# Kernel optimization log

Hardware: AMD Instinct MI355X
Metric: run time of the kernel (lower is better)

The kernel has to match this reference:

```python
import jax, jax.numpy as jnp
import numpy as np

INPUT_DIM = 1024
HIDDEN_DIM = 64   # per-head dim
NUM_HEADS = 16
PROJ = HIDDEN_DIM * NUM_HEADS  # 1024


def setup_inputs() -> dict:
    key = jax.random.key(0)
    ks = jax.random.split(key, 9)
    s = 1.0 / np.sqrt(INPUT_DIM)
    x = jax.random.normal(ks[0], (4, 2048, INPUT_DIM), dtype=jnp.float32)
    # Linear weights stored [in, out] (math-equivalent to torch's W.T)
    Wq = jax.random.uniform(ks[1], (INPUT_DIM, PROJ), jnp.float32, -s, s)
    bq = jax.random.uniform(ks[2], (PROJ,), jnp.float32, -s, s)
    Wk = jax.random.uniform(ks[3], (INPUT_DIM, PROJ), jnp.float32, -s, s)
    bk = jax.random.uniform(ks[4], (PROJ,), jnp.float32, -s, s)
    Wv = jax.random.uniform(ks[5], (INPUT_DIM, PROJ), jnp.float32, -s, s)
    bv = jax.random.uniform(ks[6], (PROJ,), jnp.float32, -s, s)
    sf = 1.0 / np.sqrt(PROJ)
    Wf = jax.random.uniform(ks[7], (PROJ, HIDDEN_DIM), jnp.float32, -sf, sf)
    bf = jax.random.uniform(ks[8], (HIDDEN_DIM,), jnp.float32, -sf, sf)
    return {"x": x, "Wq": Wq, "bq": bq, "Wk": Wk, "bk": bk,
            "Wv": Wv, "bv": bv, "Wf": Wf, "bf": bf}


def reference(x, Wq, bq, Wk, bk, Wv, bv, Wf, bf):
    B, S, _ = x.shape
    def split_heads(t):  # [B,S,H*D] -> [B,H,S,D]
        return t.reshape(B, S, NUM_HEADS, HIDDEN_DIM).transpose(0, 2, 1, 3)
    q = split_heads(x @ Wq + bq)
    k = split_heads(x @ Wk + bk)
    v = split_heads(x @ Wv + bv)
    scale = 1.0 / jnp.sqrt(jnp.float32(HIDDEN_DIM))
    scores = jnp.einsum('bhqd,bhkd->bhqk', q, k) * scale  # [B,H,S,S]
    weights = jax.nn.softmax(scores, axis=-1)
    ctx = jnp.einsum('bhqk,bhkd->bhqd', weights, v)
    ctx = ctx.transpose(0, 2, 1, 3).reshape(B, S, PROJ)
    return ctx @ Wf + bf  # [B,S,HIDDEN_DIM]
```

## Files before the change

kernel.cpp:

```cpp
#include <hip/hip_runtime.h>
#include <math.h>

#define S_LEN 2048
#define NH 16
#define HD 64
#define DMODEL 1024
#define BATCH 4
#define M_TOT (BATCH * S_LEN)

typedef __attribute__((ext_vector_type(8))) short bf16x8;
typedef __attribute__((ext_vector_type(4))) float f32x4;

#define CK 0.18033688f

__device__ __forceinline__ unsigned short f2bf_rne(float f) {
    unsigned u = __float_as_uint(f);
    u += 0x7fffu + ((u >> 16) & 1u);
    return (unsigned short)(u >> 16);
}

__device__ __forceinline__ void gld16(unsigned short* lds, const unsigned short* g) {
    __builtin_amdgcn_global_load_lds(
        (const __attribute__((address_space(1))) void*)g,
        (__attribute__((address_space(3))) void*)lds, 16, 0, 0);
}

__global__ __launch_bounds__(256) void cvt_fused(
    const float* __restrict__ x,
    const float* __restrict__ Wq, const float* __restrict__ Wk,
    const float* __restrict__ Wv, const float* __restrict__ Wf,
    unsigned short* __restrict__ xb, unsigned short* __restrict__ WT)
{
    const int z = blockIdx.z;
    const int tid = threadIdx.x;

    if (z < 4) {
        if (z == 3 && blockIdx.x > 0) return;
        const float* W = (z == 0) ? Wq : (z == 1) ? Wk : (z == 2) ? Wv : Wf;
        const int ncol = (z == 3) ? 64 : DMODEL;
        unsigned short* out = WT + (size_t)z * DMODEL * DMODEL;

        __shared__ float Lt[64][65];
        const int r0 = blockIdx.y * 64;
        const int c0 = blockIdx.x * 64;

        #pragma unroll
        for (int p = 0; p < 4; p++) {
            int row = (tid >> 4) + p * 16;
            int c4 = (tid & 15) * 4;
            float4 v = *(const float4*)(W + (size_t)(r0 + row) * ncol + c0 + c4);
            Lt[row][c4 + 0] = v.x; Lt[row][c4 + 1] = v.y;
            Lt[row][c4 + 2] = v.z; Lt[row][c4 + 3] = v.w;
        }
        __syncthreads();
        #pragma unroll
        for (int p = 0; p < 4; p++) {
            int nr = (tid >> 4) + p * 16;
            int kc = (tid & 15) * 4;
            unsigned short t[4];
            #pragma unroll
            for (int j = 0; j < 4; j++) t[j] = f2bf_rne(Lt[kc + j][nr]);
            *(uint2*)(out + (size_t)(c0 + nr) * DMODEL + r0 + kc) = *(uint2*)t;
        }
    } else {
        const int zz = z - 4;
        const int gtid = (blockIdx.y * 16 + blockIdx.x) * 256 + tid;
        #pragma unroll
        for (int it = 0; it < 2; it++) {
            #pragma unroll
            for (int k = 0; k < 4; k++) {
                size_t i = ((size_t)((zz * 8 + it * 4 + k) * 65536) + gtid) * 4;
                float4 v = *(const float4*)(x + i);
                unsigned short t[4];
                t[0] = f2bf_rne(v.x); t[1] = f2bf_rne(v.y);
                t[2] = f2bf_rne(v.z); t[3] = f2bf_rne(v.w);
                *(uint2*)(xb + i) = *(uint2*)t;
            }
        }
    }
}

__global__ __launch_bounds__(512) void qkv_fused_mfma(
    const unsigned short* __restrict__ xb,
    const unsigned short* __restrict__ WT,
    const float* __restrict__ bq, const float* __restrict__ bk,
    const float* __restrict__ bv,
    unsigned short* __restrict__ Qb, unsigned short* __restrict__ Kb,
    unsigned short* __restrict__ Vtb)
{
    __shared__ __align__(16) unsigned short Ws[3][24 * 512];

    const int lin = blockIdx.x;
    const int xcd = lin & 7;
    const int s   = lin >> 3;
    const int rb  = xcd * 4 + (s & 3);
    const int ocb = s >> 2;

    const int tid = threadIdx.x;
    const int lane = tid & 63, w = tid >> 6;
    const int quad = lane >> 4, l15 = lane & 15;

    const int R0  = rb * 256;
    const int OC0 = ocb * 64;

    const unsigned short* gW0 = WT +
        (size_t)(OC0 + (w >> 1) * 16 + l15) * DMODEL + (w & 1) * 32 + quad * 8;
    const unsigned short* gW1 = gW0 + (size_t)DMODEL * DMODEL;
    const unsigned short* gW2 = gW1 + (size_t)DMODEL * DMODEL;
    const unsigned short* gx0 = xb +
        (size_t)(R0 + w * 32 + l15) * DMODEL + quad * 8;
    const unsigned short* gx1 = gx0 + (size_t)16 * DMODEL;

    f32x4 acc[3][4][2];
    #pragma unroll
    for (int z = 0; z < 3; z++)
        #pragma unroll
        for (int i = 0; i < 4; i++)
            #pragma unroll
            for (int j = 0; j < 2; j++)
                #pragma unroll
                for (int c = 0; c < 4; c++) acc[z][i][j][c] = 0.f;

#define QKV_STAGEW(BUF, K)  do {                                       \
        gld16(Ws[BUF] + (0 * 8 + w) * 512, gW0 + (K));                 \
        gld16(Ws[BUF] + (1 * 8 + w) * 512, gW1 + (K));                 \
        gld16(Ws[BUF] + (2 * 8 + w) * 512, gW2 + (K));                 \
    } while (0)

#define QKV_LOADX(XF, K)  do {                                         \
        XF[0][0] = *(const bf16x8*)(gx0 + (K));                        \
        XF[0][1] = *(const bf16x8*)(gx0 + (K) + 32);                   \
        XF[1][0] = *(const bf16x8*)(gx1 + (K));                        \
        XF[1][1] = *(const bf16x8*)(gx1 + (K) + 32);                   \
    } while (0)

#define QKV_COMPUTE(BUF, XF)  do {                                     \
        _Pragma("unroll")                                              \
        for (int sl = 0; sl < 2; sl++) {                               \
            _Pragma("unroll")                                          \
            for (int z = 0; z < 3; z++) {                              \
                bf16x8 af[4];                                          \
                _Pragma("unroll")                                      \
                for (int i = 0; i < 4; i++)                            \
                    af[i] = *(const bf16x8*)&Ws[BUF][(z * 8 + i * 2 + sl) * 512 + lane * 8]; \
                if (z != 2) {                                          \
                    _Pragma("unroll")                                  \
                    for (int i = 0; i < 4; i++)                        \
                        _Pragma("unroll")                              \
                        for (int j = 0; j < 2; j++)                    \
                            acc[z][i][j] = __builtin_amdgcn_mfma_f32_16x16x32_bf16( \
                                af[i], XF[j][sl], acc[z][i][j], 0, 0, 0); \
                } else {                                               \
                    _Pragma("unroll")                                  \
                    for (int i = 0; i < 4; i++)                        \
                        _Pragma("unroll")                              \
                        for (int j = 0; j < 2; j++)                    \
                            acc[2][i][j] = __builtin_amdgcn_mfma_f32_16x16x32_bf16( \
                                XF[j][sl], af[i], acc[2][i][j], 0, 0, 0); \
                }                                                      \
            }                                                          \
        }                                                              \
    } while (0)

    bf16x8 xA[2][2], xB[2][2];

    QKV_STAGEW(0, 0);
    QKV_LOADX(xA, 0);
    QKV_STAGEW(1, 64);

    int b0 = 0;
    #pragma unroll 1
    for (int tt = 0; tt < 16; tt += 2) {
        const int b1 = (b0 + 1 == 3) ? 0 : b0 + 1;
        const int b2 = (b1 + 1 == 3) ? 0 : b1 + 1;

        asm volatile("s_waitcnt vmcnt(3)" ::: "memory");
        __builtin_amdgcn_s_barrier();
        if (tt < 15) QKV_LOADX(xB, (tt + 1) * 64);
        if (tt < 14) QKV_STAGEW(b2, (tt + 2) * 64);
        QKV_COMPUTE(b0, xA);

        if (tt < 14) asm volatile("s_waitcnt vmcnt(3)" ::: "memory");
        else         asm volatile("s_waitcnt vmcnt(0)" ::: "memory");
        __builtin_amdgcn_s_barrier();
        if (tt < 14) QKV_LOADX(xA, (tt + 2) * 64);
        if (tt < 13) QKV_STAGEW(b0, (tt + 3) * 64);
        QKV_COMPUTE(b1, xB);

        b0 = b2;
    }
#undef QKV_STAGEW
#undef QKV_LOADX
#undef QKV_COMPUTE

    #pragma unroll
    for (int z = 0; z < 2; z++) {
        unsigned short* out = (z == 0) ? Qb : Kb;
        const float* bias = (z == 0) ? bq : bk;
        const float qs = (z == 0) ? CK : 1.0f;
        #pragma unroll
        for (int i = 0; i < 4; i++) {
            int oc = OC0 + i * 16 + quad * 4;
            float4 bv4 = *(const float4*)&bias[oc];
            #pragma unroll
            for (int j = 0; j < 2; j++) {
                int row = R0 + w * 32 + j * 16 + l15;
                unsigned short t4[4];
                t4[0] = f2bf_rne((acc[z][i][j][0] + bv4.x) * qs);
                t4[1] = f2bf_rne((acc[z][i][j][1] + bv4.y) * qs);
                t4[2] = f2bf_rne((acc[z][i][j][2] + bv4.z) * qs);
                t4[3] = f2bf_rne((acc[z][i][j][3] + bv4.w) * qs);
                *(uint2*)(out + (size_t)row * DMODEL + oc) = *(uint2*)t4;
            }
        }
    }
    {
        const int b = R0 >> 11;
        const int sbase = (R0 & 2047) + w * 32;
        #pragma unroll
        for (int i = 0; i < 4; i++) {
            int oc = OC0 + i * 16 + l15;
            float bvv = bv[oc];
            #pragma unroll
            for (int j = 0; j < 2; j++) {
                int sq = sbase + j * 16 + quad * 4;
                unsigned short t4[4];
                t4[0] = f2bf_rne(acc[2][i][j][0] + bvv);
                t4[1] = f2bf_rne(acc[2][i][j][1] + bvv);
                t4[2] = f2bf_rne(acc[2][i][j][2] + bvv);
                t4[3] = f2bf_rne(acc[2][i][j][3] + bvv);
                *(uint2*)(Vtb + (size_t)(b * DMODEL + oc) * S_LEN + sq) = *(uint2*)t4;
            }
        }
    }
}

__global__ __launch_bounds__(512, 4) void flash_attn_mfma(
    const unsigned short* __restrict__ Qg,
    const unsigned short* __restrict__ Kg,
    const unsigned short* __restrict__ Vtg,
    unsigned short* __restrict__ ctxb)
{
    __shared__ __align__(16) unsigned short Ks[16 * 512];
    __shared__ __align__(16) unsigned short Vs[16 * 512];
    __shared__ __align__(16) unsigned short Ps[16 * 512];

    const int tid  = threadIdx.x;
    const int lane = tid & 63, w = tid >> 6;
    const int quad = lane >> 4, l15 = lane & 15;

    const int lin = blockIdx.x;
    const int xcd = lin & 7;
    const int s   = lin >> 3;
    const int bh  = xcd + 8 * (s >> 3);
    const int qblk = s & 7;
    const int b = bh >> 4, h = bh & 15;
    const int r0 = qblk * 256;

    bf16x8 qf[2][2];
    #pragma unroll
    for (int nt = 0; nt < 2; nt++)
        #pragma unroll
        for (int ds = 0; ds < 2; ds++)
            qf[nt][ds] = *(const bf16x8*)(Qg +
                (size_t)(b * S_LEN + r0 + w * 32 + nt * 16 + l15) * DMODEL +
                h * HD + ds * 32 + quad * 8);

    const int sw = w & 3;
    const unsigned short* gK = Kg +
        (size_t)(b * S_LEN + sw * 32 + l15) * DMODEL + h * HD + quad * 8;
    const unsigned short* gV = Vtg +
        ((size_t)(bh * HD + sw * 16 + l15)) * S_LEN + quad * 8;

    f32x4 O[2][4], lsum[2];
    #pragma unroll
    for (int rt = 0; rt < 2; rt++) {
        #pragma unroll
        for (int c = 0; c < 4; c++) lsum[rt][c] = 0.f;
        #pragma unroll
        for (int dt = 0; dt < 4; dt++)
            #pragma unroll
            for (int c = 0; c < 4; c++) O[rt][dt][c] = 0.f;
    }

    f32x4 zero4;
    #pragma unroll
    for (int c = 0; c < 4; c++) zero4[c] = 0.f;
    bf16x8 ones;
    #pragma unroll
    for (int c = 0; c < 8; c++) ones[c] = (short)0x3F80;

    for (int st = 0; st < S_LEN / 128; st++) {
        __syncthreads();
        if (w < 4) {
            gld16(Ks + (w * 4 + 0) * 512, gK);
            gld16(Ks + (w * 4 + 1) * 512, gK + 32);
            gld16(Ks + (w * 4 + 2) * 512, gK + (size_t)16 * DMODEL);
            gld16(Ks + (w * 4 + 3) * 512, gK + (size_t)16 * DMODEL + 32);
            gK += (size_t)128 * DMODEL;
        } else {
            gld16(Vs + (sw * 4 + 0) * 512, gV);
            gld16(Vs + (sw * 4 + 1) * 512, gV + 32);
            gld16(Vs + (sw * 4 + 2) * 512, gV + 64);
            gld16(Vs + (sw * 4 + 3) * 512, gV + 96);
            gV += 128;
        }
        __syncthreads();

        #pragma unroll
        for (int r = 0; r < 4; r++) {
            f32x4 sc[2][2];
            {
                bf16x8 kf0 = *(const bf16x8*)&Ks[((r * 2 + 0) * 2 + 0) * 512 + lane * 8];
                bf16x8 kf1 = *(const bf16x8*)&Ks[((r * 2 + 1) * 2 + 0) * 512 + lane * 8];
                sc[0][0] = __builtin_amdgcn_mfma_f32_16x16x32_bf16(kf0, qf[0][0], zero4, 0, 0, 0);
                sc[0][1] = __builtin_amdgcn_mfma_f32_16x16x32_bf16(kf0, qf[1][0], zero4, 0, 0, 0);
                sc[1][0] = __builtin_amdgcn_mfma_f32_16x16x32_bf16(kf1, qf[0][0], zero4, 0, 0, 0);
                sc[1][1] = __builtin_amdgcn_mfma_f32_16x16x32_bf16(kf1, qf[1][0], zero4, 0, 0, 0);
                kf0 = *(const bf16x8*)&Ks[((r * 2 + 0) * 2 + 1) * 512 + lane * 8];
                kf1 = *(const bf16x8*)&Ks[((r * 2 + 1) * 2 + 1) * 512 + lane * 8];
                sc[0][0] = __builtin_amdgcn_mfma_f32_16x16x32_bf16(kf0, qf[0][1], sc[0][0], 0, 0, 0);
                sc[0][1] = __builtin_amdgcn_mfma_f32_16x16x32_bf16(kf0, qf[1][1], sc[0][1], 0, 0, 0);
                sc[1][0] = __builtin_amdgcn_mfma_f32_16x16x32_bf16(kf1, qf[0][1], sc[1][0], 0, 0, 0);
                sc[1][1] = __builtin_amdgcn_mfma_f32_16x16x32_bf16(kf1, qf[1][1], sc[1][1], 0, 0, 0);
            }

            #pragma unroll
            for (int nt = 0; nt < 2; nt++) {
                #pragma unroll
                for (int mt = 0; mt < 2; mt++) {
                    unsigned u[4];
                    #pragma unroll
                    for (int c = 0; c < 4; c++)
                        u[c] = __float_as_uint(__builtin_amdgcn_exp2f(sc[mt][nt][c]));
                    uint2 pk;
                    pk.x = __builtin_amdgcn_perm(u[1], u[0], 0x07060302u);
                    pk.y = __builtin_amdgcn_perm(u[3], u[2], 0x07060302u);
                    int off = (w * 2 + nt) * 512 + (mt * 2 + (quad >> 1)) * 128 +
                              l15 * 8 + (quad & 1) * 4;
                    *(uint2*)&Ps[off] = pk;
                }
            }

            bf16x8 pf0 = *(const bf16x8*)&Ps[(w * 2 + 0) * 512 + lane * 8];
            bf16x8 pf1 = *(const bf16x8*)&Ps[(w * 2 + 1) * 512 + lane * 8];
            lsum[0] = __builtin_amdgcn_mfma_f32_16x16x32_bf16(pf0, ones, lsum[0], 0, 0, 0);
            lsum[1] = __builtin_amdgcn_mfma_f32_16x16x32_bf16(pf1, ones, lsum[1], 0, 0, 0);
            #pragma unroll
            for (int dt = 0; dt < 4; dt++) {
                bf16x8 vf = *(const bf16x8*)&Vs[(dt * 4 + r) * 512 + lane * 8];
                O[0][dt] = __builtin_amdgcn_mfma_f32_16x16x32_bf16(pf0, vf, O[0][dt], 0, 0, 0);
                O[1][dt] = __builtin_amdgcn_mfma_f32_16x16x32_bf16(pf1, vf, O[1][dt], 0, 0, 0);
            }
        }
    }

    const size_t srow = (size_t)(b * S_LEN + r0 + w * 32);
    #pragma unroll
    for (int rt = 0; rt < 2; rt++) {
        #pragma unroll
        for (int reg = 0; reg < 4; reg++) {
            float li = 1.0f / lsum[rt][reg];
            size_t rowoff = (srow + rt * 16 + quad * 4 + reg) * DMODEL + h * HD + l15;
            #pragma unroll
            for (int dt = 0; dt < 4; dt++)
                ctxb[rowoff + dt * 16] = f2bf_rne(O[rt][dt][reg] * li);
        }
    }
}

__global__ __launch_bounds__(512) void out_proj_mfma(
    const unsigned short* __restrict__ ctxb,
    const unsigned short* __restrict__ WfT,
    const float* __restrict__ bfb,
    float* __restrict__ out)
{
    __shared__ float Red[8 * 1024];

    const int tid = threadIdx.x;
    const int lane = tid & 63, w = tid >> 6;
    const int quad = lane >> 4, l15 = lane & 15;
    const int m0 = blockIdx.x * 16;

    const unsigned short* pA = ctxb + (size_t)(m0 + l15) * DMODEL + w * 128 + quad * 8;
    const unsigned short* pB = WfT + (size_t)l15 * DMODEL + w * 128 + quad * 8;

    f32x4 acc[4];
    #pragma unroll
    for (int j = 0; j < 4; j++)
        #pragma unroll
        for (int c = 0; c < 4; c++) acc[j][c] = 0.f;

    #pragma unroll
    for (int k0 = 0; k0 < 128; k0 += 32) {
        bf16x8 af = *(const bf16x8*)(pA + k0);
        #pragma unroll
        for (int j = 0; j < 4; j++) {
            bf16x8 bfr = *(const bf16x8*)(pB + (size_t)j * 16 * DMODEL + k0);
            acc[j] = __builtin_amdgcn_mfma_f32_16x16x32_bf16(af, bfr, acc[j], 0, 0, 0);
        }
    }

    #pragma unroll
    for (int j = 0; j < 4; j++)
        #pragma unroll
        for (int reg = 0; reg < 4; reg++)
            Red[w * 1024 + lane * 16 + j * 4 + reg] = acc[j][reg];
    __syncthreads();

    const int row = tid >> 5;
    const int c0  = (tid & 31) * 2;
    float2 o;
    float* op = &o.x;
    #pragma unroll
    for (int cc = 0; cc < 2; cc++) {
        int col = c0 + cc;
        int idx = ((row >> 2) * 16 + (col & 15)) * 16 + (col >> 4) * 4 + (row & 3);
        float s = 0.f;
        #pragma unroll
        for (int wv = 0; wv < 8; wv++) s += Red[wv * 1024 + idx];
        op[cc] = s + bfb[col];
    }
    *(float2*)(out + (size_t)(m0 + row) * HD + c0) = o;
}

extern "C" void kernel_launch(void* const* d_in, const int* in_sizes, int n_in,
                              void* d_out, int out_size, void* d_ws, size_t ws_size,
                              hipStream_t stream)
{
    (void)in_sizes; (void)n_in; (void)out_size; (void)ws_size;
    const float* x  = (const float*)d_in[0];
    const float* Wq = (const float*)d_in[1];
    const float* bq = (const float*)d_in[2];
    const float* Wk = (const float*)d_in[3];
    const float* bk = (const float*)d_in[4];
    const float* Wv = (const float*)d_in[5];
    const float* bv = (const float*)d_in[6];
    const float* Wf = (const float*)d_in[7];
    const float* bf = (const float*)d_in[8];
    float* out = (float*)d_out;

    char* wsb = (char*)d_ws;
    unsigned short* xb   = (unsigned short*)wsb;
    unsigned short* ctxb = (unsigned short*)wsb;
    unsigned short* WT   = xb + (size_t)M_TOT * DMODEL;
    unsigned short* WfT  = WT + (size_t)3 * DMODEL * DMODEL;
    unsigned short* Qb   = (unsigned short*)(wsb + (size_t)32 * 1024 * 1024);
    unsigned short* Kb   = Qb + (size_t)M_TOT * DMODEL;
    unsigned short* Vtb  = Kb + (size_t)M_TOT * DMODEL;

    cvt_fused<<<dim3(16, 16, 8), 256, 0, stream>>>(x, Wq, Wk, Wv, Wf, xb, WT);
    qkv_fused_mfma<<<dim3(512), 512, 0, stream>>>(xb, WT, bq, bk, bv, Qb, Kb, Vtb);
    flash_attn_mfma<<<dim3(512), 512, 0, stream>>>(Qb, Kb, Vtb, ctxb);
    out_proj_mfma<<<dim3(M_TOT / 16), 512, 0, stream>>>(ctxb, WfT, bf, out);
}
```

Measured before the change: 256.1 us.

## Fuse output projection into flash attention epilogue with atomic accumulation

Removes the separate output-projection kernel: each attention block stages its normalized per-head context tile in swizzled LDS, multiplies it by that head's slice of Wf with MFMA, and atomically adds the partial result into the fp32 output, which is zeroed by a memset beforehand. This avoids writing and rereading the bf16 context tensor and one launch. In exchange it adds 16-way atomic contention per output element, extra LDS that may lower occupancy, and nondeterministic summation order.

```diff
diff --git a/kernel.cpp b/kernel.cpp
--- a/kernel.cpp
+++ b/kernel.cpp
@@ -239,11 +239,14 @@
     const unsigned short* __restrict__ Qg,
     const unsigned short* __restrict__ Kg,
     const unsigned short* __restrict__ Vtg,
-    unsigned short* __restrict__ ctxb)
+    const unsigned short* __restrict__ WfT,
+    const float* __restrict__ bfb,
+    float* __restrict__ out)
 {
     __shared__ __align__(16) unsigned short Ks[16 * 512];
     __shared__ __align__(16) unsigned short Vs[16 * 512];
     __shared__ __align__(16) unsigned short Ps[16 * 512];
+    __shared__ __align__(16) unsigned short Cs[256 * 64];
 
     const int tid  = threadIdx.x;
     const int lane = tid & 63, w = tid >> 6;
@@ -355,73 +358,67 @@
         }
     }
 
-    const size_t srow = (size_t)(b * S_LEN + r0 + w * 32);
     #pragma unroll
     for (int rt = 0; rt < 2; rt++) {
         #pragma unroll
         for (int reg = 0; reg < 4; reg++) {
             float li = 1.0f / lsum[rt][reg];
-            size_t rowoff = (srow + rt * 16 + quad * 4 + reg) * DMODEL + h * HD + l15;
-            #pragma unroll
-            for (int dt = 0; dt < 4; dt++)
-                ctxb[rowoff + dt * 16] = f2bf_rne(O[rt][dt][reg] * li);
-        }
-    }
-}
-
-__global__ __launch_bounds__(512) void out_proj_mfma(
-    const unsigned short* __restrict__ ctxb,
-    const unsigned short* __restrict__ WfT,
-    const float* __restrict__ bfb,
-    float* __restrict__ out)
-{
-    __shared__ float Red[8 * 1024];
-
-    const int tid = threadIdx.x;
-    const int lane = tid & 63, w = tid >> 6;
-    const int quad = lane >> 4, l15 = lane & 15;
-    const int m0 = blockIdx.x * 16;
-
-    const unsigned short* pA = ctxb + (size_t)(m0 + l15) * DMODEL + w * 128 + quad * 8;
-    const unsigned short* pB = WfT + (size_t)l15 * DMODEL + w * 128 + quad * 8;
-
-    f32x4 acc[4];
-    #pragma unroll
-    for (int j = 0; j < 4; j++)
-        #pragma unroll
-        for (int c = 0; c < 4; c++) acc[j][c] = 0.f;
-
-    #pragma unroll
-    for (int k0 = 0; k0 < 128; k0 += 32) {
-        bf16x8 af = *(const bf16x8*)(pA + k0);
-        #pragma unroll
-        for (int j = 0; j < 4; j++) {
-            bf16x8 bfr = *(const bf16x8*)(pB + (size_t)j * 16 * DMODEL + k0);
-            acc[j] = __builtin_amdgcn_mfma_f32_16x16x32_bf16(af, bfr, acc[j], 0, 0, 0);
-        }
-    }
-
-    #pragma unroll
-    for (int j = 0; j < 4; j++)
-        #pragma unroll
-        for (int reg = 0; reg < 4; reg++)
-            Red[w * 1024 + lane * 16 + j * 4 + reg] = acc[j][reg];
+            int r = w * 32 + rt * 16 + quad * 4 + reg;
+            int swz = (r & 7) << 4;
+            #pragma unroll
+            for (int dt = 0; dt < 4; dt++) {
+                int byte_off = (r * 128 + (dt * 16 + l15) * 2) ^ swz;
+                *(unsigned short*)((char*)Cs + byte_off) = f2bf_rne(O[rt][dt][reg] * li);
+            }
+        }
+    }
     __syncthreads();
 
-    const int row = tid >> 5;
-    const int c0  = (tid & 31) * 2;
-    float2 o;
-    float* op = &o.x;
-    #pragma unroll
-    for (int cc = 0; cc < 2; cc++) {
-        int col = c0 + cc;
-        int idx = ((row >> 2) * 16 + (col & 15)) * 16 + (col >> 4) * 4 + (row & 3);
-        float s = 0.f;
-        #pragma unroll
-        for (int wv = 0; wv < 8; wv++) s += Red[wv * 1024 + idx];
-        op[cc] = s + bfb[col];
-    }
-    *(float2*)(out + (size_t)(m0 + row) * HD + c0) = o;
+    f32x4 acc2[2][4];
+    #pragma unroll
+    for (int mt = 0; mt < 2; mt++)
+        #pragma unroll
+        for (int nt = 0; nt < 4; nt++)
+            #pragma unroll
+            for (int c = 0; c < 4; c++) acc2[mt][nt][c] = 0.f;
+
+    bf16x8 bw[4][2];
+    #pragma unroll
+    for (int nt = 0; nt < 4; nt++)
+        #pragma unroll
+        for (int ks = 0; ks < 2; ks++)
+            bw[nt][ks] = *(const bf16x8*)(WfT +
+                (size_t)(nt * 16 + l15) * DMODEL + h * HD + ks * 32 + quad * 8);
+
+    #pragma unroll
+    for (int mt = 0; mt < 2; mt++) {
+        int row = w * 32 + mt * 16 + l15;
+        int swz = (row & 7) << 4;
+        #pragma unroll
+        for (int ks = 0; ks < 2; ks++) {
+            bf16x8 a = *(const bf16x8*)((char*)Cs +
+                (((row * 128) + ks * 64 + quad * 16) ^ swz));
+            #pragma unroll
+            for (int nt = 0; nt < 4; nt++)
+                acc2[mt][nt] = __builtin_amdgcn_mfma_f32_16x16x32_bf16(
+                    a, bw[nt][ks], acc2[mt][nt], 0, 0, 0);
+        }
+    }
+
+    const size_t srow = (size_t)(b * S_LEN + r0 + w * 32);
+    #pragma unroll
+    for (int mt = 0; mt < 2; mt++) {
+        #pragma unroll
+        for (int nt = 0; nt < 4; nt++) {
+            int oc = nt * 16 + l15;
+            float bias = (h == 0) ? bfb[oc] : 0.f;
+            #pragma unroll
+            for (int reg = 0; reg < 4; reg++) {
+                size_t row = srow + mt * 16 + quad * 4 + reg;
+                atomicAdd(out + row * HD + oc, acc2[mt][nt][reg] + bias);
+            }
+        }
+    }
 }
 
 extern "C" void kernel_launch(void* const* d_in, const int* in_sizes, int n_in,
@@ -442,15 +439,14 @@
 
     char* wsb = (char*)d_ws;
     unsigned short* xb   = (unsigned short*)wsb;
-    unsigned short* ctxb = (unsigned short*)wsb;
     unsigned short* WT   = xb + (size_t)M_TOT * DMODEL;
     unsigned short* WfT  = WT + (size_t)3 * DMODEL * DMODEL;
     unsigned short* Qb   = (unsigned short*)(wsb + (size_t)32 * 1024 * 1024);
     unsigned short* Kb   = Qb + (size_t)M_TOT * DMODEL;
     unsigned short* Vtb  = Kb + (size_t)M_TOT * DMODEL;
 
+    hipMemsetAsync(out, 0, (size_t)M_TOT * HD * sizeof(float), stream);
     cvt_fused<<<dim3(16, 16, 8), 256, 0, stream>>>(x, Wq, Wk, Wv, Wf, xb, WT);
     qkv_fused_mfma<<<dim3(512), 512, 0, stream>>>(xb, WT, bq, bk, bv, Qb, Kb, Vtb);
-    flash_attn_mfma<<<dim3(512), 512, 0, stream>>>(Qb, Kb, Vtb, ctxb);
-    out_proj_mfma<<<dim3(M_TOT / 16), 512, 0, stream>>>(ctxb, WfT, bf, out);
-}
+    flash_attn_mfma<<<dim3(512), 512, 0, stream>>>(Qb, Kb, Vtb, WfT, bf, out);
+}
```

After: 269.4 us. +5.2%, slower.
